# Kernel tuning notes

Measured on AMD Instinct MI355X. Metric: run time of the kernel, lower is better.

The kernel has to match this reference:

```python
import jax, jax.numpy as jnp
import numpy as np

N, E, F_IN, HID, HEADS, NG, NC = 50000, 800000, 128, 64, 4, 64, 10
NEG_SLOPE = 0.2


def gat_conv(h_in, src, dst, W, att_src, att_dst, bias, heads, out_ch, concat, num_nodes):
    # h_in: [N, Fin]; W: [Fin, heads*out_ch]; att_*: [heads, out_ch]; bias: [heads*out_ch] or [out_ch]
    h = (h_in @ W).reshape(num_nodes, heads, out_ch)            # [N,H,C]
    a_src = jnp.sum(h * att_src, axis=-1)                        # [N,H]
    a_dst = jnp.sum(h * att_dst, axis=-1)                        # [N,H]
    alpha = jax.nn.leaky_relu(a_src[src] + a_dst[dst], NEG_SLOPE)  # [Etot,H]
    # softmax over incoming edges per destination node
    amax = jax.ops.segment_max(alpha, dst, num_segments=num_nodes)
    amax = jnp.where(jnp.isfinite(amax), amax, 0.0)
    ex = jnp.exp(alpha - amax[dst])
    denom = jax.ops.segment_sum(ex, dst, num_segments=num_nodes)
    w = ex / (denom[dst] + 1e-16)                                # [Etot,H]
    msg = h[src] * w[:, :, None]                                 # [Etot,H,C]
    out = jax.ops.segment_sum(msg, dst, num_segments=num_nodes)  # [N,H,C]
    out = out.reshape(num_nodes, heads * out_ch) if concat else out.mean(axis=1)
    return out + bias


def setup_inputs() -> dict:
    key = jax.random.key(0)
    ks = jax.random.split(key, 20)
    s = lambda k, shp, f: (jax.random.normal(k, shp, jnp.float32) * f)
    return {
        "x": jax.random.normal(ks[0], (N, F_IN), jnp.float32),
        "edge_index": jax.random.randint(ks[1], (2, E), 0, N, jnp.int32),
        "batch": jax.random.randint(ks[2], (N,), 0, NG, jnp.int32),
        "W_proj": s(ks[3], (F_IN, HID), 0.05), "b_proj": jnp.zeros((HID,), jnp.float32),
        "W1": s(ks[4], (HID, HEADS * HID), 0.05),
        "att_src1": s(ks[5], (HEADS, HID), 0.1), "att_dst1": s(ks[6], (HEADS, HID), 0.1),
        "b1": jnp.zeros((HEADS * HID,), jnp.float32),
        "W2": s(ks[7], (HEADS * HID, HID), 0.05),
        "att_src2": s(ks[8], (1, HID), 0.1), "att_dst2": s(ks[9], (1, HID), 0.1),
        "b2": jnp.zeros((HID,), jnp.float32),
        "W_fc1": s(ks[10], (HID, HID // 2), 0.05), "b_fc1": jnp.zeros((HID // 2,), jnp.float32),
        "W_fc2": s(ks[11], (HID // 2, NC), 0.05), "b_fc2": jnp.zeros((NC,), jnp.float32),
    }


def reference(x, edge_index, batch, W_proj, b_proj, W1, att_src1, att_dst1, b1,
              W2, att_src2, att_dst2, b2, W_fc1, b_fc1, W_fc2, b_fc2):
    n = x.shape[0]
    loops = jnp.arange(n, dtype=edge_index.dtype)  # PyG GATConv add_self_loops=True
    src = jnp.concatenate([edge_index[0], loops])
    dst = jnp.concatenate([edge_index[1], loops])
    h = jax.nn.relu(x @ W_proj + b_proj)                                  # feature_proj + relu
    h = gat_conv(h, src, dst, W1, att_src1, att_dst1, b1, HEADS, HID, True, n)
    h = jax.nn.leaky_relu(h, NEG_SLOPE)                                    # dropout = identity (eval)
    h = gat_conv(h, src, dst, W2, att_src2, att_dst2, b2, 1, HID, False, n)
    h = jax.nn.leaky_relu(h, NEG_SLOPE)
    cnt = jax.ops.segment_sum(jnp.ones((n,), h.dtype), batch, num_segments=NG)
    gmean = jax.ops.segment_sum(h, batch, num_segments=NG) / jnp.maximum(cnt, 1.0)[:, None]
    gmax = jax.ops.segment_max(h, batch, num_segments=NG)
    gmax = jnp.where(jnp.isfinite(gmax), gmax, 0.0)
    g = gmean + gmax
    g = jax.nn.relu(g @ W_fc1 + b_fc1)
    return jax.nn.log_softmax(g @ W_fc2 + b_fc2, axis=1)
```

## Files before the change

### kernel.cpp

```cpp
#include <hip/hip_runtime.h>
#include <math.h>

#define NN 50000
#define EE 800000
#define ET 850000
#define FIN 128
#define HD 64
#define NH 4
#define NGR 64
#define NCL 10
#define NEG 0.2f
#define NBK 196
#define ECH 831

typedef unsigned short u16;
typedef unsigned char u8;
typedef unsigned int u32;
typedef __attribute__((ext_vector_type(8))) short short8;
typedef __attribute__((ext_vector_type(4))) float f32x4;

__device__ __forceinline__ float lrelu(float x){ return x > 0.f ? x : NEG * x; }

__device__ __forceinline__ float wsum(float v){
#pragma unroll
  for (int o = 32; o > 0; o >>= 1) v += __shfl_xor(v, o, 64);
  return v;
}
__device__ __forceinline__ float wmax(float v){
#pragma unroll
  for (int o = 32; o > 0; o >>= 1) v = fmaxf(v, __shfl_xor(v, o, 64));
  return v;
}
__device__ __forceinline__ int wsumi(int v){
#pragma unroll
  for (int o = 32; o > 0; o >>= 1) v += __shfl_xor(v, o, 64);
  return v;
}
__device__ __forceinline__ int esrc(const int* ei, int e){ return e < EE ? ei[e] : e - EE; }
__device__ __forceinline__ int edst(const int* ei, int e){ return e < EE ? ei[EE + e] : e - EE; }

__device__ __forceinline__ unsigned f2key(float f){
  unsigned u = __float_as_uint(f);
  return (u & 0x80000000u) ? ~u : (u | 0x80000000u);
}
__device__ __forceinline__ float key2f(unsigned k){
  return (k & 0x80000000u) ? __uint_as_float(k & 0x7fffffffu) : __uint_as_float(~k);
}

__device__ __forceinline__ u16 f2b(float f){
  u32 u = __float_as_uint(f);
  u32 r = (u + 0x7FFFu + ((u >> 16) & 1u)) >> 16;
  return (u16)r;
}
__device__ __forceinline__ float b2f(u16 b){ return __uint_as_float(((u32)b) << 16); }
__device__ __forceinline__ u32 pkbf16(float lo, float hi){
  u32 r;
  asm("v_cvt_pk_bf16_f32 %0, %1, %2" : "=v"(r) : "v"(lo), "v"(hi));
  return r;
}
__device__ __forceinline__ u8 f2fp8(float f){
  return (u8)__builtin_amdgcn_cvt_pk_fp8_f32(f, 0.f, 0, false);
}
__device__ __forceinline__ int rl(int v, int idx){ return __builtin_amdgcn_readlane(v, idx); }
__device__ __forceinline__ float rlf(float v, int idx){
  return __uint_as_float((u32)__builtin_amdgcn_readlane((int)__float_as_uint(v), idx));
}

__global__ __launch_bounds__(256) void k_b1hist(const int* __restrict__ ei, int* __restrict__ bcnt){
  __shared__ int lc[NBK];
  int t = threadIdx.x, blk = blockIdx.x;
  for (int i = t; i < NBK; i += 256) lc[i] = 0;
  __syncthreads();
#pragma unroll
  for (int k = 0; k < 4; ++k){
    int e = blk*1024 + k*256 + t;
    if (e < ET) atomicAdd(&lc[edst(ei, e) >> 8], 1);
  }
  __syncthreads();
  for (int i = t; i < NBK; i += 256) bcnt[i*ECH + blk] = lc[i];
}

__global__ __launch_bounds__(256) void k_bscana(const int* __restrict__ bcnt, int* __restrict__ btot){
  int b = blockIdx.x, t = threadIdx.x;
  int s = 0;
  for (int j = t; j < ECH; j += 256) s += bcnt[b*ECH + j];
  s = wsumi(s);
  __shared__ int w4[4];
  if ((t & 63) == 0) w4[t >> 6] = s;
  __syncthreads();
  if (t == 0) btot[b] = w4[0] + w4[1] + w4[2] + w4[3];
}

__global__ __launch_bounds__(256) void k_bscanb(const int* __restrict__ bcnt, const int* __restrict__ btot,
                                                int* __restrict__ boff, int* __restrict__ bb){
  int b = blockIdx.x, t = threadIdx.x;
  int pv = (t < b) ? btot[t] : 0;
  int r = wsumi(pv);
  __shared__ int w4[4];
  if ((t & 63) == 0) w4[t >> 6] = r;
  __syncthreads();
  int base = w4[0] + w4[1] + w4[2] + w4[3];
  if (t == 0) bb[b] = base;
  __shared__ int s[256];
  int carry = 0;
  for (int j0 = 0; j0 < ECH; j0 += 256){
    int j = j0 + t;
    int v = (j < ECH) ? bcnt[b*ECH + j] : 0;
    s[t] = v; __syncthreads();
    for (int d = 1; d < 256; d <<= 1){
      int xv = (t >= d) ? s[t-d] : 0;
      __syncthreads();
      s[t] += xv;
      __syncthreads();
    }
    int excl = s[t] - v;
    if (j < ECH) boff[b*ECH + j] = base + carry + excl;
    int tot = s[255];
    __syncthreads();
    carry += tot;
  }
}

__global__ __launch_bounds__(256) void k_b1scat(const int* __restrict__ ei, const int* __restrict__ boff,
                                                u32* __restrict__ packed){
  __shared__ int lpos[NBK];
  int t = threadIdx.x, blk = blockIdx.x;
  for (int i = t; i < NBK; i += 256) lpos[i] = boff[i*ECH + blk];
  __syncthreads();
#pragma unroll
  for (int k = 0; k < 4; ++k){
    int e = blk*1024 + k*256 + t;
    if (e < ET){
      int d = edst(ei, e);
      int s = esrc(ei, e);
      int slot = atomicAdd(&lpos[d >> 8], 1);
      packed[slot] = ((u32)(d & 255) << 16) | (u32)s;
    }
  }
}

__global__ __launch_bounds__(256) void k_phf2(
            const u32* __restrict__ packed, const int* __restrict__ btot, const int* __restrict__ bb,
            int* __restrict__ off, u16* __restrict__ csrc,
            const float* __restrict__ x, const float* __restrict__ Wp, const float* __restrict__ bp,
            const float* __restrict__ W1, const float* __restrict__ as1, const float* __restrict__ ad1,
            u8* __restrict__ h1f8, float* __restrict__ a_s, float* __restrict__ a_d, int gb){
  __shared__ u16 As[64*(FIN+8)];
  __shared__ u16 h0s[64*(HD+8)];
  __shared__ int hc[256];
  __shared__ int sc[256];
  __shared__ int pp[256];
  int t = threadIdx.x;
  int bid = blockIdx.x;
  if (bid >= gb){
    int b = bid - gb;
    int e0 = bb[b];
    int cntb = btot[b];
    hc[t] = 0;
    __syncthreads();
    for (int i = t; i < cntb; i += 256){
      u32 p = packed[e0 + i];
      atomicAdd(&hc[p >> 16], 1);
    }
    __syncthreads();
    int v = hc[t];
    sc[t] = v; __syncthreads();
    for (int d = 1; d < 256; d <<= 1){
      int xv = (t >= d) ? sc[t-d] : 0;
      __syncthreads();
      sc[t] += xv;
      __syncthreads();
    }
    int excl = sc[t] - v;
    int node = b*256 + t;
    if (node < NN) off[node] = e0 + excl;
    if (b == 0 && t == 0) off[NN] = ET;
    pp[t] = excl;
    __syncthreads();
    for (int i = t; i < cntb; i += 256){
      u32 p = packed[e0 + i];
      int slot = atomicAdd(&pp[p >> 16], 1);
      csrc[(size_t)e0 + slot] = (u16)(p & 0xFFFFu);
    }
    return;
  }
  constexpr int LDK1 = FIN + 8;
  constexpr int LDH  = HD + 8;
  int w = t >> 6, l = t & 63;
  int l16 = l & 15, kg = l >> 4;

  short8 bfp[4];
#pragma unroll
  for (int kt = 0; kt < 4; ++kt){
    short8 v;
#pragma unroll
    for (int j = 0; j < 8; ++j) v[j] = (short)f2b(Wp[(size_t)(kt*32 + kg*8 + j)*HD + w*16 + l16]);
    bfp[kt] = v;
  }
  short8 bf1[2*4];
#pragma unroll
  for (int kt = 0; kt < 2; ++kt)
#pragma unroll
    for (int nt = 0; nt < 4; ++nt){
      short8 v;
#pragma unroll
      for (int j = 0; j < 8; ++j) v[j] = (short)f2b(W1[(size_t)(kt*32 + kg*8 + j)*256 + w*64 + nt*16 + l16]);
      bf1[kt*4 + nt] = v;
    }
  float bv = bp[w*16 + l16];
  float asv[4], adv[4];
#pragma unroll
  for (int nt = 0; nt < 4; ++nt){
    asv[nt] = as1[w*64 + nt*16 + l16];
    adv[nt] = ad1[w*64 + nt*16 + l16];
  }

  for (int ch = 0; ch < 2; ++ch){
    int nb = (bid*2 + ch)*64;
    if (nb >= NN) break;
    __syncthreads();
    for (int u = t; u < 64*16; u += 256){
      int r = u >> 4, c = u & 15;
      int n = nb + r;
      uint4 v = make_uint4(0u,0u,0u,0u);
      if (n < NN){
        float4 f0 = *(const float4*)&x[(size_t)n*FIN + c*8];
        float4 f1 = *(const float4*)&x[(size_t)n*FIN + c*8 + 4];
        v = make_uint4(pkbf16(f0.x,f0.y), pkbf16(f0.z,f0.w), pkbf16(f1.x,f1.y), pkbf16(f1.z,f1.w));
      }
      *(uint4*)&As[r*LDK1 + c*8] = v;
    }
    __syncthreads();
#pragma unroll
    for (int rt = 0; rt < 4; ++rt){
      short8 afp[4];
#pragma unroll
      for (int kt = 0; kt < 4; ++kt)
        afp[kt] = *(const short8*)&As[(rt*16 + l16)*LDK1 + kt*32 + kg*8];
      f32x4 acc = (f32x4){0.f,0.f,0.f,0.f};
#pragma unroll
      for (int kt = 0; kt < 4; ++kt)
        acc = __builtin_amdgcn_mfma_f32_16x16x32_bf16(afp[kt], bfp[kt], acc, 0, 0, 0);
#pragma unroll
      for (int r4 = 0; r4 < 4; ++r4)
        h0s[(rt*16 + kg*4 + r4)*LDH + w*16 + l16] = f2b(fmaxf(acc[r4] + bv, 0.f));
    }
    __syncthreads();
#pragma unroll
    for (int rt = 0; rt < 4; ++rt){
      short8 af[2];
#pragma unroll
      for (int kt = 0; kt < 2; ++kt)
        af[kt] = *(const short8*)&h0s[(rt*16 + l16)*LDH + kt*32 + kg*8];
      f32x4 acc[4];
#pragma unroll
      for (int nt = 0; nt < 4; ++nt){
        acc[nt] = (f32x4){0.f,0.f,0.f,0.f};
#pragma unroll
        for (int kt = 0; kt < 2; ++kt)
          acc[nt] = __builtin_amdgcn_mfma_f32_16x16x32_bf16(af[kt], bf1[kt*4 + nt], acc[nt], 0, 0, 0);
      }
      int rbase = nb + rt*16 + kg*4;
#pragma unroll
      for (int nt = 0; nt < 4; ++nt)
#pragma unroll
        for (int r4 = 0; r4 < 4; ++r4){
          int n = rbase + r4;
          if (n < NN) h1f8[(size_t)n*256 + w*64 + nt*16 + l16] = f2fp8(acc[nt][r4]);
        }
#pragma unroll
      for (int r4 = 0; r4 < 4; ++r4){
        float ps = 0.f, pd = 0.f;
#pragma unroll
        for (int nt = 0; nt < 4; ++nt){
          ps = fmaf(acc[nt][r4], asv[nt], ps);
          pd = fmaf(acc[nt][r4], adv[nt], pd);
        }
#pragma unroll
        for (int o = 1; o < 16; o <<= 1){
          ps += __shfl_xor(ps, o, 64);
          pd += __shfl_xor(pd, o, 64);
        }
        int n = rbase + r4;
        if (l16 == 0 && n < NN){ a_s[n*NH + w] = ps; a_d[n*NH + w] = pd; }
      }
    }
  }
}

template<int K, int NOUT, int CPW>
__device__ __forceinline__ void gemm_body2(int bid, u16* As, float* sred,
            const u16* __restrict__ A, const float* __restrict__ Bf,
            const float* __restrict__ att_s, const float* __restrict__ att_d,
            u16* __restrict__ C, float* __restrict__ a_s, float* __restrict__ a_d){
  constexpr int KT = K/32;
  constexpr int LDK = K + 8;
  int t = threadIdx.x, w = t >> 6, l = t & 63;
  int c0 = w*CPW;
  int l16 = l & 15, kg = l >> 4;

  short8 bf[KT];
#pragma unroll
  for (int kt = 0; kt < KT; ++kt){
    int kbase = kt*32 + kg*8;
    int col = c0 + l16;
    short8 v;
#pragma unroll
    for (int j = 0; j < 8; ++j) v[j] = (short)f2b(Bf[(size_t)(kbase + j)*NOUT + col]);
    bf[kt] = v;
  }
  float asv = att_s[c0 + l16], adv = att_d[c0 + l16];

  for (int ch = 0; ch < 2; ++ch){
    int nb = (bid*2 + ch)*64;
    if (nb >= NN) break;
    __syncthreads();
    constexpr int UPR = K/8;
    for (int u = t; u < 64*UPR; u += 256){
      int r = u / UPR, c = u % UPR;
      int n = nb + r;
      uint4 v = make_uint4(0u,0u,0u,0u);
      if (n < NN) v = *(const uint4*)&A[(size_t)n*K + c*8];
      *(uint4*)&As[r*LDK + c*8] = v;
    }
    __syncthreads();
#pragma unroll
    for (int rt = 0; rt < 4; ++rt){
      short8 af[KT];
#pragma unroll
      for (int kt = 0; kt < KT; ++kt)
        af[kt] = *(const short8*)&As[(rt*16 + l16)*LDK + kt*32 + kg*8];
      f32x4 acc = (f32x4){0.f,0.f,0.f,0.f};
#pragma unroll
      for (int kt = 0; kt < KT; ++kt)
        acc = __builtin_amdgcn_mfma_f32_16x16x32_bf16(af[kt], bf[kt], acc, 0, 0, 0);
      int rbase = nb + rt*16 + kg*4;
#pragma unroll
      for (int r4 = 0; r4 < 4; ++r4){
        int n = rbase + r4;
        if (n < NN) C[(size_t)n*NOUT + c0 + l16] = f2b(acc[r4]);
      }
#pragma unroll
      for (int r4 = 0; r4 < 4; ++r4){
        float ps = acc[r4]*asv;
        float pd = acc[r4]*adv;
#pragma unroll
        for (int o = 1; o < 16; o <<= 1){
          ps += __shfl_xor(ps, o, 64);
          pd += __shfl_xor(pd, o, 64);
        }
        if (l16 == 0){
          int row = rt*16 + kg*4 + r4;
          sred[(w*64 + row)*2]     = ps;
          sred[(w*64 + row)*2 + 1] = pd;
        }
      }
    }
    __syncthreads();
    if (t < 64){
      int n = nb + t;
      if (n < NN){
        float s = sred[t*2] + sred[(64+t)*2] + sred[(128+t)*2] + sred[(192+t)*2];
        float d = sred[t*2+1] + sred[(64+t)*2+1] + sred[(128+t)*2+1] + sred[(192+t)*2+1];
        a_s[n] = s; a_d[n] = d;
      }
    }
  }
}

__global__ __launch_bounds__(256) void k_feat2(const u16* __restrict__ h1outb, const float* __restrict__ W2,
            const float* __restrict__ as2, const float* __restrict__ ad2,
            u16* __restrict__ h2b, float* __restrict__ a_s, float* __restrict__ a_d){
  __shared__ u16 As[64*(256+8)];
  __shared__ float sred[4*64*2];
  gemm_body2<256, 64, 16>(blockIdx.x, As, sred, h1outb, W2, as2, ad2, h2b, a_s, a_d);
}

__global__ __launch_bounds__(256) void k_gat1(const u8* __restrict__ h1f8, const float* __restrict__ a_s,
                       const float* __restrict__ a_d, const int* __restrict__ off,
                       const u16* __restrict__ csrc, const float* __restrict__ b1,
                       u16* __restrict__ h1outb){
  __shared__ float lw[4][4][68];
  int wv = threadIdx.x >> 6, l = threadIdx.x & 63;
  int n = blockIdx.x*4 + wv;
  if (n >= NN) return;
  int e0 = off[n], e1 = off[n+1], deg = e1 - e0;
  int j16 = l & 15, h = l >> 4;
  float adst = a_d[n*NH + h];
  float acc0 = 0.f, acc1 = 0.f, acc2 = 0.f, acc3 = 0.f;
  const u8* base = h1f8 + 4*l;

#define GAT1_FMA8(wrd, wq) { \
  acc0 = fmaf(__builtin_amdgcn_cvt_f32_fp8((int)(wrd), 0), wq, acc0); \
  acc1 = fmaf(__builtin_amdgcn_cvt_f32_fp8((int)(wrd), 1), wq, acc1); \
  acc2 = fmaf(__builtin_amdgcn_cvt_f32_fp8((int)(wrd), 2), wq, acc2); \
  acc3 = fmaf(__builtin_amdgcn_cvt_f32_fp8((int)(wrd), 3), wq, acc3); }

  if (deg <= 64){
    int sreg[4]; float wreg[4];
#pragma unroll
    for (int c = 0; c < 4; ++c){
      int idx = c*16 + j16;
      int s = (idx < deg) ? (int)csrc[e0 + idx] : 0;
      sreg[c] = s;
      wreg[c] = (idx < deg) ? lrelu(a_s[s*NH + h] + adst) : -3.0e38f;
    }
    float m = fmaxf(fmaxf(wreg[0], wreg[1]), fmaxf(wreg[2], wreg[3]));
#pragma unroll
    for (int o2 = 1; o2 < 16; o2 <<= 1) m = fmaxf(m, __shfl_xor(m, o2, 64));
    float se = 0.f;
#pragma unroll
    for (int c = 0; c < 4; ++c){
      int idx = c*16 + j16;
      float wc = (idx < deg) ? __expf(wreg[c] - m) : 0.f;
      wreg[c] = wc; se += wc;
    }
#pragma unroll
    for (int o2 = 1; o2 < 16; o2 <<= 1) se += __shfl_xor(se, o2, 64);
    float inv = 1.f / (se + 1e-16f);
#pragma unroll
    for (int c = 0; c < 4; ++c) lw[wv][h][c*16 + j16] = wreg[c] * inv;

#pragma unroll
    for (int c = 0; c < 4; ++c){
      int cbase = c*16;
      if (cbase < deg){
        int cnt = deg - cbase; if (cnt > 16) cnt = 16;
        int j2 = 0;
        for (; j2 + 8 <= cnt; j2 += 8){
          float4 wqa = *(const float4*)&lw[wv][h][cbase + j2];
          float4 wqb = *(const float4*)&lw[wv][h][cbase + j2 + 4];
          int s0 = rl(sreg[c], j2),   s1 = rl(sreg[c], j2+1);
          int s2 = rl(sreg[c], j2+2), s3 = rl(sreg[c], j2+3);
          int s4 = rl(sreg[c], j2+4), s5 = rl(sreg[c], j2+5);
          int s6 = rl(sreg[c], j2+6), s7 = rl(sreg[c], j2+7);
          u32 w0 = *(const u32*)(base + (size_t)(u32)s0*256);
          u32 w1 = *(const u32*)(base + (size_t)(u32)s1*256);
          u32 w2 = *(const u32*)(base + (size_t)(u32)s2*256);
          u32 w3 = *(const u32*)(base + (size_t)(u32)s3*256);
          u32 w4 = *(const u32*)(base + (size_t)(u32)s4*256);
          u32 w5 = *(const u32*)(base + (size_t)(u32)s5*256);
          u32 w6 = *(const u32*)(base + (size_t)(u32)s6*256);
          u32 w7 = *(const u32*)(base + (size_t)(u32)s7*256);
          GAT1_FMA8(w0, wqa.x) GAT1_FMA8(w1, wqa.y) GAT1_FMA8(w2, wqa.z) GAT1_FMA8(w3, wqa.w)
          GAT1_FMA8(w4, wqb.x) GAT1_FMA8(w5, wqb.y) GAT1_FMA8(w6, wqb.z) GAT1_FMA8(w7, wqb.w)
        }
        for (; j2 + 4 <= cnt; j2 += 4){
          float4 wq = *(const float4*)&lw[wv][h][cbase + j2];
          int s0 = rl(sreg[c], j2),   s1 = rl(sreg[c], j2+1);
          int s2 = rl(sreg[c], j2+2), s3 = rl(sreg[c], j2+3);
          u32 w0 = *(const u32*)(base + (size_t)(u32)s0*256);
          u32 w1 = *(const u32*)(base + (size_t)(u32)s1*256);
          u32 w2 = *(const u32*)(base + (size_t)(u32)s2*256);
          u32 w3 = *(const u32*)(base + (size_t)(u32)s3*256);
          GAT1_FMA8(w0, wq.x) GAT1_FMA8(w1, wq.y) GAT1_FMA8(w2, wq.z) GAT1_FMA8(w3, wq.w)
        }
        for (; j2 < cnt; ++j2){
          float wqs = lw[wv][h][cbase + j2];
          int s = rl(sreg[c], j2);
          u32 wd = *(const u32*)(base + (size_t)(u32)s*256);
          GAT1_FMA8(wd, wqs)
        }
      }
    }
  } else {
    float m = -3.0e38f;
    for (int i = e0 + j16; i < e1; i += 16){
      int s = csrc[i];
      m = fmaxf(m, lrelu(a_s[s*NH + h] + adst));
    }
#pragma unroll
    for (int o2 = 1; o2 < 16; o2 <<= 1) m = fmaxf(m, __shfl_xor(m, o2, 64));
    float se = 0.f;
    for (int i = e0 + j16; i < e1; i += 16){
      int s = csrc[i];
      se += __expf(lrelu(a_s[s*NH + h] + adst) - m);
    }
#pragma unroll
    for (int o2 = 1; o2 < 16; o2 <<= 1) se += __shfl_xor(se, o2, 64);
    float inv = 1.f / (se + 1e-16f);
    for (int i = e0; i < e1; ++i){
      int s = csrc[i];
      float wq = __expf(lrelu(a_s[s*NH + h] + adst) - m) * inv;
      u32 wd = *(const u32*)(base + (size_t)(u32)s*256);
      GAT1_FMA8(wd, wq)
    }
  }
  float4 bv = *(const float4*)&b1[4*l];
  u32 lo = pkbf16(lrelu(acc0 + bv.x), lrelu(acc1 + bv.y));
  u32 hi = pkbf16(lrelu(acc2 + bv.z), lrelu(acc3 + bv.w));
  *(uint2*)&h1outb[(size_t)n*256 + 4*l] = make_uint2(lo, hi);
}

__global__ __launch_bounds__(256) void k_gat2(const u16* __restrict__ h2b, const float* __restrict__ a_s,
                       const float* __restrict__ a_d, const int* __restrict__ off,
                       const u16* __restrict__ csrc, const float* __restrict__ b2v,
                       float* __restrict__ h2out){
  int wv = threadIdx.x >> 6, l = threadIdx.x & 63;
  int n = blockIdx.x*4 + wv;
  if (n >= NN) return;
  int e0 = off[n], e1 = off[n+1], deg = e1 - e0;
  float adst = a_d[n];
  if (deg <= 64){
    int sA = 0; float alA = -3.0e38f;
    if (l < deg){
      sA = (int)csrc[e0 + l];
      alA = lrelu(a_s[sA] + adst);
    }
    float m = wmax(alA);
    float wA = (l < deg) ? __expf(alA - m) : 0.f;
    float se = wsum(wA);
    wA *= 1.f / (se + 1e-16f);
    float acc = 0.f;
    int idx = 0;
    for (; idx + 8 <= deg; idx += 8){
      int s0 = rl(sA, idx),   s1 = rl(sA, idx+1);
      int s2 = rl(sA, idx+2), s3 = rl(sA, idx+3);
      int s4 = rl(sA, idx+4), s5 = rl(sA, idx+5);
      int s6 = rl(sA, idx+6), s7 = rl(sA, idx+7);
      float w0 = rlf(wA, idx),   w1 = rlf(wA, idx+1);
      float w2 = rlf(wA, idx+2), w3 = rlf(wA, idx+3);
      float w4 = rlf(wA, idx+4), w5 = rlf(wA, idx+5);
      float w6 = rlf(wA, idx+6), w7 = rlf(wA, idx+7);
      float v0 = b2f(h2b[(size_t)(u32)s0*HD + l]);
      float v1 = b2f(h2b[(size_t)(u32)s1*HD + l]);
      float v2 = b2f(h2b[(size_t)(u32)s2*HD + l]);
      float v3 = b2f(h2b[(size_t)(u32)s3*HD + l]);
      float v4 = b2f(h2b[(size_t)(u32)s4*HD + l]);
      float v5 = b2f(h2b[(size_t)(u32)s5*HD + l]);
      float v6 = b2f(h2b[(size_t)(u32)s6*HD + l]);
      float v7 = b2f(h2b[(size_t)(u32)s7*HD + l]);
      acc = fmaf(v0, w0, acc); acc = fmaf(v1, w1, acc);
      acc = fmaf(v2, w2, acc); acc = fmaf(v3, w3, acc);
      acc = fmaf(v4, w4, acc); acc = fmaf(v5, w5, acc);
      acc = fmaf(v6, w6, acc); acc = fmaf(v7, w7, acc);
    }
    for (; idx < deg; ++idx){
      int s = rl(sA, idx);
      float w = rlf(wA, idx);
      acc = fmaf(b2f(h2b[(size_t)(u32)s*HD + l]), w, acc);
    }
    h2out[(size_t)n*HD + l] = lrelu(acc + b2v[l]);
  } else {
    float m = -3.0e38f;
    for (int i = e0 + l; i < e1; i += 64){
      int s = csrc[i];
      m = fmaxf(m, lrelu(a_s[s] + adst));
    }
    m = wmax(m);
    float se = 0.f;
    for (int i = e0 + l; i < e1; i += 64){
      int s = csrc[i];
      se += __expf(lrelu(a_s[s] + adst) - m);
    }
    se = wsum(se);
    float inv = 1.f / (se + 1e-16f);
    float acc = 0.f;
    for (int i = e0; i < e1; ++i){
      int s = csrc[i];
      acc += b2f(h2b[(size_t)s*HD + l]) * __expf(lrelu(a_s[s] + adst) - m);
    }
    h2out[(size_t)n*HD + l] = lrelu(acc*inv + b2v[l]);
  }
}


__global__ void k_pool(const float* __restrict__ h2out, const int* __restrict__ batch,
                       float* __restrict__ gsum, unsigned* __restrict__ gmaxk, int* __restrict__ gcnt){
  __shared__ float ssum[NGR*HD];
  __shared__ unsigned smax[NGR*HD];
  __shared__ int scnt[NGR];
  int t = threadIdx.x;
  for (int i = t; i < NGR*HD; i += 256){ ssum[i] = 0.f; smax[i] = 0u; }
  if (t < NGR) scnt[t] = 0;
  __syncthreads();
  int wv = t >> 6, lane = t & 63;
  for (int n = blockIdx.x*4 + wv; n < NN; n += gridDim.x*4){
    int g = batch[n];
    float v = h2out[(size_t)n*HD + lane];
    atomicAdd(&ssum[g*HD + lane], v);
    atomicMax(&smax[g*HD + lane], f2key(v));
    if (lane == 0) atomicAdd(&scnt[g], 1);
  }
  __syncthreads();
  for (int i = t; i < NGR*HD; i += 256){
    atomicAdd(&gsum[i], ssum[i]);
    atomicMax(&gmaxk[i], smax[i]);
  }
  if (t < NGR) atomicAdd(&gcnt[t], scnt[t]);
}


__global__ void k_final(const float* __restrict__ gsum, const unsigned* __restrict__ gmaxk,
                        const int* __restrict__ gcnt,
                        const float* __restrict__ Wf1, const float* __restrict__ bf1,
                        const float* __restrict__ Wf2, const float* __restrict__ bf2,
                        float* __restrict__ out){
  int g = blockIdx.x, t = threadIdx.x;
  __shared__ float gv[HD];
  __shared__ float f1[32];
  __shared__ float lg[NCL];
  int c = gcnt[g];
  float dn = fmaxf((float)c, 1.f);
  float mean = gsum[g*HD + t] / dn;
  float mx = (c > 0) ? key2f(gmaxk[g*HD + t]) : 0.f;
  gv[t] = mean + mx;
  __syncthreads();
  if (t < 32){
    float a = bf1[t];
#pragma unroll
    for (int k = 0; k < HD; ++k) a += gv[k] * Wf1[k*32 + t];
    f1[t] = a > 0.f ? a : 0.f;
  }
  __syncthreads();
  if (t < NCL){
    float a = bf2[t];
#pragma unroll
    for (int k = 0; k < 32; ++k) a += f1[k] * Wf2[k*NCL + t];
    lg[t] = a;
  }
  __syncthreads();
  if (t < NCL){
    float m = lg[0];
#pragma unroll
    for (int i = 1; i < NCL; ++i) m = fmaxf(m, lg[i]);
    float s = 0.f;
#pragma unroll
    for (int i = 0; i < NCL; ++i) s += expf(lg[i] - m);
    out[g*NCL + t] = lg[t] - m - logf(s);
  }
}

extern "C" void kernel_launch(void* const* d_in, const int* in_sizes, int n_in,
                              void* d_out, int out_size, void* d_ws, size_t ws_size,
                              hipStream_t stream) {
  const float* x   = (const float*)d_in[0];
  const int*   ei  = (const int*)d_in[1];
  const int*   bat = (const int*)d_in[2];
  const float* Wp  = (const float*)d_in[3];
  const float* bp  = (const float*)d_in[4];
  const float* W1  = (const float*)d_in[5];
  const float* as1 = (const float*)d_in[6];
  const float* ad1 = (const float*)d_in[7];
  const float* b1  = (const float*)d_in[8];
  const float* W2  = (const float*)d_in[9];
  const float* as2 = (const float*)d_in[10];
  const float* ad2 = (const float*)d_in[11];
  const float* b2  = (const float*)d_in[12];
  const float* Wf1 = (const float*)d_in[13];
  const float* bf1 = (const float*)d_in[14];
  const float* Wf2 = (const float*)d_in[15];
  const float* bf2 = (const float*)d_in[16];
  float* out = (float*)d_out;

  char* base = (char*)d_ws;
  size_t o = 0;
  auto alloc = [&](size_t elems) -> char* {
    char* p = base + o*4;
    o += (elems + 63) & ~(size_t)63;
    return p;
  };
  u8*    h1f8   = (u8*)alloc(3200000);
  u16*   h1outb = (u16*)alloc(6400000);
  u16*   h2b    = (u16*)alloc(1600000);
  float* h2out  = (float*)alloc(3200000);
  float* a_s1   = (float*)alloc(200000);
  float* a_d1   = (float*)alloc(200000);
  float* a_s2   = (float*)alloc(50000);
  float* a_d2   = (float*)alloc(50000);
  int*   off    = (int*)alloc(50001);
  int*   bcnt   = (int*)alloc(NBK*ECH);
  int*   boff   = (int*)alloc(NBK*ECH);
  int*   btot   = (int*)alloc(256);
  int*   bb     = (int*)alloc(256);
  u32*   packed = (u32*)alloc(850000);
  u16*   csrc   = (u16*)alloc(425000);
  float* gsum   = (float*)alloc(NGR*HD);
  unsigned* gmaxk = (unsigned*)alloc(NGR*HD);
  int*   gcnt   = (int*)alloc(NGR);

  const int GB  = (NN + 127) / 128;
  const int WB  = (NN + 3) / 4;

  hipMemsetAsync(gsum, 0, (NGR*HD*2 + 64)*sizeof(int), stream);

  k_b1hist<<<ECH, 256, 0, stream>>>(ei, bcnt);
  k_bscana<<<NBK, 256, 0, stream>>>(bcnt, btot);
  k_bscanb<<<NBK, 256, 0, stream>>>(bcnt, btot, boff, bb);
  k_b1scat<<<ECH, 256, 0, stream>>>(ei, boff, packed);

  k_phf2<<<GB + NBK, 256, 0, stream>>>(packed, btot, bb, off, csrc,
                                       x, Wp, bp, W1, as1, ad1, h1f8, a_s1, a_d1, GB);

  k_gat1<<<WB, 256, 0, stream>>>(h1f8, a_s1, a_d1, off, csrc, b1, h1outb);

  k_feat2<<<GB, 256, 0, stream>>>(h1outb, W2, as2, ad2, h2b, a_s2, a_d2);
  k_gat2<<<WB, 256, 0, stream>>>(h2b, a_s2, a_d2, off, csrc, b2, h2out);

  k_pool<<<256, 256, 0, stream>>>(h2out, bat, gsum, gmaxk, gcnt);

  k_final<<<NGR, 64, 0, stream>>>(gsum, gmaxk, gcnt, Wf1, bf1, Wf2, bf2, out);
}
```

Before: 175.9 us.

## Split feature GEMM chain across histogram and scatter kernels; use packed fp8 convert

```diff
diff --git a/kernel.cpp b/kernel.cpp
--- a/kernel.cpp
+++ b/kernel.cpp
@@ -18,6 +18,7 @@
 typedef unsigned int u32;
 typedef __attribute__((ext_vector_type(8))) short short8;
 typedef __attribute__((ext_vector_type(4))) float f32x4;
+typedef __attribute__((ext_vector_type(2))) float f32x2;
 
 __device__ __forceinline__ float lrelu(float x){ return x > 0.f ? x : NEG * x; }
 
@@ -66,9 +67,127 @@
   return __uint_as_float((u32)__builtin_amdgcn_readlane((int)__float_as_uint(v), idx));
 }
 
-__global__ __launch_bounds__(256) void k_b1hist(const int* __restrict__ ei, int* __restrict__ bcnt){
+__device__ __forceinline__ void gemm_chain(int gbid, u16* As, u16* h0s,
+            const float* __restrict__ x, const float* __restrict__ Wp, const float* __restrict__ bp,
+            const float* __restrict__ W1, const float* __restrict__ as1, const float* __restrict__ ad1,
+            u8* __restrict__ h1f8, float* __restrict__ a_s, float* __restrict__ a_d){
+  constexpr int LDK1 = FIN + 8;
+  constexpr int LDH  = HD + 8;
+  int t = threadIdx.x, w = t >> 6, l = t & 63;
+  int l16 = l & 15, kg = l >> 4;
+
+  short8 bfp[4];
+#pragma unroll
+  for (int kt = 0; kt < 4; ++kt){
+    short8 v;
+#pragma unroll
+    for (int j = 0; j < 8; ++j) v[j] = (short)f2b(Wp[(size_t)(kt*32 + kg*8 + j)*HD + w*16 + l16]);
+    bfp[kt] = v;
+  }
+  short8 bf1[2*4];
+#pragma unroll
+  for (int kt = 0; kt < 2; ++kt)
+#pragma unroll
+    for (int nt = 0; nt < 4; ++nt){
+      short8 v;
+#pragma unroll
+      for (int j = 0; j < 8; ++j) v[j] = (short)f2b(W1[(size_t)(kt*32 + kg*8 + j)*256 + w*64 + nt*16 + l16]);
+      bf1[kt*4 + nt] = v;
+    }
+  float bv = bp[w*16 + l16];
+  float asv[4], adv[4];
+#pragma unroll
+  for (int nt = 0; nt < 4; ++nt){
+    asv[nt] = as1[w*64 + nt*16 + l16];
+    adv[nt] = ad1[w*64 + nt*16 + l16];
+  }
+
+  for (int ch = 0; ch < 2; ++ch){
+    int nb = (gbid*2 + ch)*64;
+    if (nb >= NN) break;
+    __syncthreads();
+    for (int u = t; u < 64*16; u += 256){
+      int r = u >> 4, c = u & 15;
+      int n = nb + r;
+      uint4 v = make_uint4(0u,0u,0u,0u);
+      if (n < NN){
+        float4 f0 = *(const float4*)&x[(size_t)n*FIN + c*8];
+        float4 f1 = *(const float4*)&x[(size_t)n*FIN + c*8 + 4];
+        v = make_uint4(pkbf16(f0.x,f0.y), pkbf16(f0.z,f0.w), pkbf16(f1.x,f1.y), pkbf16(f1.z,f1.w));
+      }
+      *(uint4*)&As[r*LDK1 + c*8] = v;
+    }
+    __syncthreads();
+#pragma unroll
+    for (int rt = 0; rt < 4; ++rt){
+      short8 afp[4];
+#pragma unroll
+      for (int kt = 0; kt < 4; ++kt)
+        afp[kt] = *(const short8*)&As[(rt*16 + l16)*LDK1 + kt*32 + kg*8];
+      f32x4 acc = (f32x4){0.f,0.f,0.f,0.f};
+#pragma unroll
+      for (int kt = 0; kt < 4; ++kt)
+        acc = __builtin_amdgcn_mfma_f32_16x16x32_bf16(afp[kt], bfp[kt], acc, 0, 0, 0);
+#pragma unroll
+      for (int r4 = 0; r4 < 4; ++r4)
+        h0s[(rt*16 + kg*4 + r4)*LDH + w*16 + l16] = f2b(fmaxf(acc[r4] + bv, 0.f));
+    }
+    __syncthreads();
+#pragma unroll
+    for (int rt = 0; rt < 4; ++rt){
+      short8 af[2];
+#pragma unroll
+      for (int kt = 0; kt < 2; ++kt)
+        af[kt] = *(const short8*)&h0s[(rt*16 + l16)*LDH + kt*32 + kg*8];
+      f32x4 acc[4];
+#pragma unroll
+      for (int nt = 0; nt < 4; ++nt){
+        acc[nt] = (f32x4){0.f,0.f,0.f,0.f};
+#pragma unroll
+        for (int kt = 0; kt < 2; ++kt)
+          acc[nt] = __builtin_amdgcn_mfma_f32_16x16x32_bf16(af[kt], bf1[kt*4 + nt], acc[nt], 0, 0, 0);
+      }
+      int rbase = nb + rt*16 + kg*4;
+#pragma unroll
+      for (int nt = 0; nt < 4; ++nt)
+#pragma unroll
+        for (int r4 = 0; r4 < 4; ++r4){
+          int n = rbase + r4;
+          if (n < NN) h1f8[(size_t)n*256 + w*64 + nt*16 + l16] = f2fp8(acc[nt][r4]);
+        }
+#pragma unroll
+      for (int r4 = 0; r4 < 4; ++r4){
+        float ps = 0.f, pd = 0.f;
+#pragma unroll
+        for (int nt = 0; nt < 4; ++nt){
+          ps = fmaf(acc[nt][r4], asv[nt], ps);
+          pd = fmaf(acc[nt][r4], adv[nt], pd);
+        }
+#pragma unroll
+        for (int o = 1; o < 16; o <<= 1){
+          ps += __shfl_xor(ps, o, 64);
+          pd += __shfl_xor(pd, o, 64);
+        }
+        int n = rbase + r4;
+        if (l16 == 0 && n < NN){ a_s[n*NH + w] = ps; a_d[n*NH + w] = pd; }
+      }
+    }
+  }
+}
+
+__global__ __launch_bounds__(256) void k_g1_hist(const int* __restrict__ ei, int* __restrict__ bcnt,
+            const float* __restrict__ x, const float* __restrict__ Wp, const float* __restrict__ bp,
+            const float* __restrict__ W1, const float* __restrict__ as1, const float* __restrict__ ad1,
+            u8* __restrict__ h1f8, float* __restrict__ a_s, float* __restrict__ a_d, int gb1){
+  __shared__ u16 As[64*(FIN+8)];
+  __shared__ u16 h0s[64*(HD+8)];
   __shared__ int lc[NBK];
-  int t = threadIdx.x, blk = blockIdx.x;
+  int b = blockIdx.x, t = threadIdx.x;
+  if (b < gb1){
+    gemm_chain(b, As, h0s, x, Wp, bp, W1, as1, ad1, h1f8, a_s, a_d);
+    return;
+  }
+  int blk = b - gb1;
   for (int i = t; i < NBK; i += 256) lc[i] = 0;
   __syncthreads();
 #pragma unroll
@@ -121,10 +240,20 @@
   }
 }
 
-__global__ __launch_bounds__(256) void k_b1scat(const int* __restrict__ ei, const int* __restrict__ boff,
-                                                u32* __restrict__ packed){
+__global__ __launch_bounds__(256) void k_g2_scat(const int* __restrict__ ei, const int* __restrict__ boff,
+            u32* __restrict__ packed,
+            const float* __restrict__ x, const float* __restrict__ Wp, const float* __restrict__ bp,
+            const float* __restrict__ W1, const float* __restrict__ as1, const float* __restrict__ ad1,
+            u8* __restrict__ h1f8, float* __restrict__ a_s, float* __restrict__ a_d, int gb2, int goff){
+  __shared__ u16 As[64*(FIN+8)];
+  __shared__ u16 h0s[64*(HD+8)];
   __shared__ int lpos[NBK];
-  int t = threadIdx.x, blk = blockIdx.x;
+  int b = blockIdx.x, t = threadIdx.x;
+  if (b < gb2){
+    gemm_chain(b + goff, As, h0s, x, Wp, bp, W1, as1, ad1, h1f8, a_s, a_d);
+    return;
+  }
+  int blk = b - gb2;
   for (int i = t; i < NBK; i += 256) lpos[i] = boff[i*ECH + blk];
   __syncthreads();
 #pragma unroll
@@ -139,152 +268,39 @@
   }
 }
 
-__global__ __launch_bounds__(256) void k_phf2(
-            const u32* __restrict__ packed, const int* __restrict__ btot, const int* __restrict__ bb,
-            int* __restrict__ off, u16* __restrict__ csrc,
-            const float* __restrict__ x, const float* __restrict__ Wp, const float* __restrict__ bp,
-            const float* __restrict__ W1, const float* __restrict__ as1, const float* __restrict__ ad1,
-            u8* __restrict__ h1f8, float* __restrict__ a_s, float* __restrict__ a_d, int gb){
-  __shared__ u16 As[64*(FIN+8)];
-  __shared__ u16 h0s[64*(HD+8)];
+__global__ __launch_bounds__(256) void k_bfin(const u32* __restrict__ packed, const int* __restrict__ btot,
+            const int* __restrict__ bb, int* __restrict__ off, u16* __restrict__ csrc){
   __shared__ int hc[256];
   __shared__ int sc[256];
   __shared__ int pp[256];
-  int t = threadIdx.x;
-  int bid = blockIdx.x;
-  if (bid >= gb){
-    int b = bid - gb;
-    int e0 = bb[b];
-    int cntb = btot[b];
-    hc[t] = 0;
-    __syncthreads();
-    for (int i = t; i < cntb; i += 256){
-      u32 p = packed[e0 + i];
-      atomicAdd(&hc[p >> 16], 1);
-    }
-    __syncthreads();
-    int v = hc[t];
-    sc[t] = v; __syncthreads();
-    for (int d = 1; d < 256; d <<= 1){
-      int xv = (t >= d) ? sc[t-d] : 0;
-      __syncthreads();
-      sc[t] += xv;
-      __syncthreads();
-    }
-    int excl = sc[t] - v;
-    int node = b*256 + t;
-    if (node < NN) off[node] = e0 + excl;
-    if (b == 0 && t == 0) off[NN] = ET;
-    pp[t] = excl;
-    __syncthreads();
-    for (int i = t; i < cntb; i += 256){
-      u32 p = packed[e0 + i];
-      int slot = atomicAdd(&pp[p >> 16], 1);
-      csrc[(size_t)e0 + slot] = (u16)(p & 0xFFFFu);
-    }
-    return;
-  }
-  constexpr int LDK1 = FIN + 8;
-  constexpr int LDH  = HD + 8;
-  int w = t >> 6, l = t & 63;
-  int l16 = l & 15, kg = l >> 4;
-
-  short8 bfp[4];
-#pragma unroll
-  for (int kt = 0; kt < 4; ++kt){
-    short8 v;
-#pragma unroll
-    for (int j = 0; j < 8; ++j) v[j] = (short)f2b(Wp[(size_t)(kt*32 + kg*8 + j)*HD + w*16 + l16]);
-    bfp[kt] = v;
-  }
-  short8 bf1[2*4];
-#pragma unroll
-  for (int kt = 0; kt < 2; ++kt)
-#pragma unroll
-    for (int nt = 0; nt < 4; ++nt){
-      short8 v;
-#pragma unroll
-      for (int j = 0; j < 8; ++j) v[j] = (short)f2b(W1[(size_t)(kt*32 + kg*8 + j)*256 + w*64 + nt*16 + l16]);
-      bf1[kt*4 + nt] = v;
-    }
-  float bv = bp[w*16 + l16];
-  float asv[4], adv[4];
-#pragma unroll
-  for (int nt = 0; nt < 4; ++nt){
-    asv[nt] = as1[w*64 + nt*16 + l16];
-    adv[nt] = ad1[w*64 + nt*16 + l16];
-  }
-
-  for (int ch = 0; ch < 2; ++ch){
-    int nb = (bid*2 + ch)*64;
-    if (nb >= NN) break;
-    __syncthreads();
-    for (int u = t; u < 64*16; u += 256){
-      int r = u >> 4, c = u & 15;
-      int n = nb + r;
-      uint4 v = make_uint4(0u,0u,0u,0u);
-      if (n < NN){
-        float4 f0 = *(const float4*)&x[(size_t)n*FIN + c*8];
-        float4 f1 = *(const float4*)&x[(size_t)n*FIN + c*8 + 4];
-        v = make_uint4(pkbf16(f0.x,f0.y), pkbf16(f0.z,f0.w), pkbf16(f1.x,f1.y), pkbf16(f1.z,f1.w));
-      }
-      *(uint4*)&As[r*LDK1 + c*8] = v;
-    }
-    __syncthreads();
-#pragma unroll
-    for (int rt = 0; rt < 4; ++rt){
-      short8 afp[4];
-#pragma unroll
-      for (int kt = 0; kt < 4; ++kt)
-        afp[kt] = *(const short8*)&As[(rt*16 + l16)*LDK1 + kt*32 + kg*8];
-      f32x4 acc = (f32x4){0.f,0.f,0.f,0.f};
-#pragma unroll
-      for (int kt = 0; kt < 4; ++kt)
-        acc = __builtin_amdgcn_mfma_f32_16x16x32_bf16(afp[kt], bfp[kt], acc, 0, 0, 0);
-#pragma unroll
-      for (int r4 = 0; r4 < 4; ++r4)
-        h0s[(rt*16 + kg*4 + r4)*LDH + w*16 + l16] = f2b(fmaxf(acc[r4] + bv, 0.f));
-    }
-    __syncthreads();
-#pragma unroll
-    for (int rt = 0; rt < 4; ++rt){
-      short8 af[2];
-#pragma unroll
-      for (int kt = 0; kt < 2; ++kt)
-        af[kt] = *(const short8*)&h0s[(rt*16 + l16)*LDH + kt*32 + kg*8];
-      f32x4 acc[4];
-#pragma unroll
-      for (int nt = 0; nt < 4; ++nt){
-        acc[nt] = (f32x4){0.f,0.f,0.f,0.f};
-#pragma unroll
-        for (int kt = 0; kt < 2; ++kt)
-          acc[nt] = __builtin_amdgcn_mfma_f32_16x16x32_bf16(af[kt], bf1[kt*4 + nt], acc[nt], 0, 0, 0);
-      }
-      int rbase = nb + rt*16 + kg*4;
-#pragma unroll
-      for (int nt = 0; nt < 4; ++nt)
-#pragma unroll
-        for (int r4 = 0; r4 < 4; ++r4){
-          int n = rbase + r4;
-          if (n < NN) h1f8[(size_t)n*256 + w*64 + nt*16 + l16] = f2fp8(acc[nt][r4]);
-        }
-#pragma unroll
-      for (int r4 = 0; r4 < 4; ++r4){
-        float ps = 0.f, pd = 0.f;
-#pragma unroll
-        for (int nt = 0; nt < 4; ++nt){
-          ps = fmaf(acc[nt][r4], asv[nt], ps);
-          pd = fmaf(acc[nt][r4], adv[nt], pd);
-        }
-#pragma unroll
-        for (int o = 1; o < 16; o <<= 1){
-          ps += __shfl_xor(ps, o, 64);
-          pd += __shfl_xor(pd, o, 64);
-        }
-        int n = rbase + r4;
-        if (l16 == 0 && n < NN){ a_s[n*NH + w] = ps; a_d[n*NH + w] = pd; }
-      }
-    }
+  int t = threadIdx.x, b = blockIdx.x;
+  int e0 = bb[b];
+  int cntb = btot[b];
+  hc[t] = 0;
+  __syncthreads();
+  for (int i = t; i < cntb; i += 256){
+    u32 p = packed[e0 + i];
+    atomicAdd(&hc[p >> 16], 1);
+  }
+  __syncthreads();
+  int v = hc[t];
+  sc[t] = v; __syncthreads();
+  for (int d = 1; d < 256; d <<= 1){
+    int xv = (t >= d) ? sc[t-d] : 0;
+    __syncthreads();
+    sc[t] += xv;
+    __syncthreads();
+  }
+  int excl = sc[t] - v;
+  int node = b*256 + t;
+  if (node < NN) off[node] = e0 + excl;
+  if (b == 0 && t == 0) off[NN] = ET;
+  pp[t] = excl;
+  __syncthreads();
+  for (int i = t; i < cntb; i += 256){
+    u32 p = packed[e0 + i];
+    int slot = atomicAdd(&pp[p >> 16], 1);
+    csrc[(size_t)e0 + slot] = (u16)(p & 0xFFFFu);
   }
 }
 
@@ -391,10 +407,10 @@
   const u8* base = h1f8 + 4*l;
 
 #define GAT1_FMA8(wrd, wq) { \
-  acc0 = fmaf(__builtin_amdgcn_cvt_f32_fp8((int)(wrd), 0), wq, acc0); \
-  acc1 = fmaf(__builtin_amdgcn_cvt_f32_fp8((int)(wrd), 1), wq, acc1); \
-  acc2 = fmaf(__builtin_amdgcn_cvt_f32_fp8((int)(wrd), 2), wq, acc2); \
-  acc3 = fmaf(__builtin_amdgcn_cvt_f32_fp8((int)(wrd), 3), wq, acc3); }
+  f32x2 lo_ = __builtin_amdgcn_cvt_pk_f32_fp8((int)(wrd), false); \
+  f32x2 hi_ = __builtin_amdgcn_cvt_pk_f32_fp8((int)(wrd), true); \
+  acc0 = fmaf(lo_.x, wq, acc0); acc1 = fmaf(lo_.y, wq, acc1); \
+  acc2 = fmaf(hi_.x, wq, acc2); acc3 = fmaf(hi_.y, wq, acc3); }
 
   if (deg <= 64){
     int sreg[4]; float wreg[4];
@@ -680,17 +696,17 @@
   int*   gcnt   = (int*)alloc(NGR);
 
   const int GB  = (NN + 127) / 128;
+  const int GB1 = 196;
+  const int GB2 = GB - GB1;
   const int WB  = (NN + 3) / 4;
 
   hipMemsetAsync(gsum, 0, (NGR*HD*2 + 64)*sizeof(int), stream);
 
-  k_b1hist<<<ECH, 256, 0, stream>>>(ei, bcnt);
+  k_g1_hist<<<GB1 + ECH, 256, 0, stream>>>(ei, bcnt, x, Wp, bp, W1, as1, ad1, h1f8, a_s1, a_d1, GB1);
   k_bscana<<<NBK, 256, 0, stream>>>(bcnt, btot);
   k_bscanb<<<NBK, 256, 0, stream>>>(bcnt, btot, boff, bb);
-  k_b1scat<<<ECH, 256, 0, stream>>>(ei, boff, packed);
-
-  k_phf2<<<GB + NBK, 256, 0, stream>>>(packed, btot, bb, off, csrc,
-                                       x, Wp, bp, W1, as1, ad1, h1f8, a_s1, a_d1, GB);
+  k_g2_scat<<<GB2 + ECH, 256, 0, stream>>>(ei, boff, packed, x, Wp, bp, W1, as1, ad1, h1f8, a_s1, a_d1, GB2, GB1);
+  k_bfin<<<NBK, 256, 0, stream>>>(packed, btot, bb, off, csrc);
 
   k_gat1<<<WB, 256, 0, stream>>>(h1f8, a_s1, a_d1, off, csrc, b1, h1outb);
 
```

Result: slower. 194.7 us (+10.7%).
